# Kernel optimization log

Hardware: AMD Instinct MI355X
Metric: run time of the kernel (lower is better)

Reference implementation:

```python
import jax, jax.numpy as jnp
import numpy as np

N_NODES = 50000


def setup_inputs() -> dict:
    key = jax.random.key(0)
    ks = jax.random.split(key, 10)
    B, N, D, H, O = 2, N_NODES, 128, 128, 10
    x = jax.random.normal(ks[0], (B, N, D), dtype=jnp.float32)
    edge_index = jax.random.randint(ks[1], (2, 800000), 0, N, dtype=jnp.int32)
    s = lambda fan_in: 1.0 / np.sqrt(fan_in)
    W  = jax.random.uniform(ks[2], (D, H), jnp.float32, -s(D), s(D))
    b  = jnp.zeros((H,), jnp.float32)
    W1 = jax.random.uniform(ks[3], (H, H // 2), jnp.float32, -s(H), s(H))
    b1 = jnp.zeros((H // 2,), jnp.float32)
    W2 = jax.random.uniform(ks[4], (H // 2, H // 4), jnp.float32, -s(H // 2), s(H // 2))
    b2 = jnp.zeros((H // 4,), jnp.float32)
    W3 = jax.random.uniform(ks[5], (H // 4, O), jnp.float32, -s(H // 4), s(H // 4))
    b3 = jnp.zeros((O,), jnp.float32)
    return {"x": x, "edge_index": edge_index, "W": W, "b": b,
            "W1": W1, "b1": b1, "W2": W2, "b2": b2, "W3": W3, "b3": b3}


def reference(x, edge_index, W, b, W1, b1, W2, b2, W3, b3):
    # GraphConvolution (Kipf): support = x @ W; out[dst] += support[src]; + b
    src, dst = edge_index[0], edge_index[1]
    support = jnp.einsum("bnd,dh->bnh", x, W)          # [B, N, H]
    msgs = support[:, src, :]                            # [B, E, H] gather
    agg = jnp.zeros_like(support).at[:, dst, :].add(msgs)  # scatter-add
    h = jax.nn.gelu(agg + b, approximate=False)          # GELU (torch default erf)
    # dropout is identity at inference (training=False)
    h = jax.nn.relu(jnp.einsum("bnh,hk->bnk", h, W1) + b1)
    h = jax.nn.relu(jnp.einsum("bnk,km->bnm", h, W2) + b2)
    h = jnp.einsum("bnm,mo->bno", h, W3) + b3            # [B, N, O]
    return h.mean(axis=1)                                # [B, O]
```

## Files before the change

kernel.cpp:

```cpp
#include <hip/hip_runtime.h>
#include <math.h>

#define NN 50000
#define DD 128
#define HH 128
#define L1 64
#define L2 32
#define OO 10

typedef short v8s __attribute__((ext_vector_type(8)));
typedef float v4f __attribute__((ext_vector_type(4)));

__device__ __forceinline__ float bf2f_lo(unsigned u) { return __uint_as_float(u << 16); }
__device__ __forceinline__ float bf2f_hi(unsigned u) { return __uint_as_float(u & 0xffff0000u); }
__device__ __forceinline__ unsigned short f2bf(float f) {
    unsigned u = __float_as_uint(f);
    return (unsigned short)((u + 0x7fffu + ((u >> 16) & 1u)) >> 16);
}
__device__ __forceinline__ float gelu_f(float v) {
    return 0.5f * v * (1.f + erff(v * 0.70710678118654752f));
}

__global__ __launch_bounds__(256) void k_wprep(
    const float* __restrict__ W, const float* __restrict__ W1,
    const float* __restrict__ W2, unsigned short* __restrict__ wtb,
    unsigned short* __restrict__ w1tb, unsigned short* __restrict__ w2tb)
{
    int i = blockIdx.x * 256 + threadIdx.x;
    if (i < 128 * 136) {
        int n = i / 136, k = i % 136;
        wtb[i] = (k < DD) ? f2bf(W[k * HH + n]) : (unsigned short)0;
    } else if (i < 128 * 136 + 64 * 136) {
        int j = i - 128 * 136;
        int n = j / 136, k = j % 136;
        w1tb[j] = (k < HH) ? f2bf(W1[k * L1 + n]) : (unsigned short)0;
    } else if (i < 128 * 136 + 64 * 136 + 32 * 72) {
        int j = i - (128 * 136 + 64 * 136);
        int n = j / 72, k = j % 72;
        w2tb[j] = (k < L1) ? f2bf(W2[k * L2 + n]) : (unsigned short)0;
    }
}

__global__ __launch_bounds__(256) void k_xcvt(
    const float* __restrict__ x, unsigned short* __restrict__ xb,
    const int* __restrict__ ei, int* __restrict__ counts, int E)
{
    const int gid = blockIdx.x * 256 + threadIdx.x;
    const int stride = gridDim.x * 256;
    const int HALF = NN * 32;
    for (int idx = gid; idx < 2 * HALF; idx += stride) {
        const int b = (idx >= HALF) ? 1 : 0;
        const int j = idx - b * HALF;
        const int n = j >> 5;
        const int c4 = j & 31;
        const float4 v = *(const float4*)(x + ((size_t)b * NN + n) * DD + c4 * 4);
        ushort4 o;
        o.x = f2bf(v.x); o.y = f2bf(v.y); o.z = f2bf(v.z); o.w = f2bf(v.w);
        *(ushort4*)(xb + ((size_t)n * 2 + b) * DD + c4 * 4) = o;
    }
    for (int e = gid; e < E; e += stride)
        atomicAdd(&counts[ei[(size_t)E + e]], 1);
}

__global__ __launch_bounds__(1024) void k_scan1(
    const int* __restrict__ counts, int* __restrict__ offsets,
    int* __restrict__ blksum, int n)
{
    __shared__ int wsum[16], woff[16];
    const int tid = threadIdx.x, lane = tid & 63, wv = tid >> 6;
    const int i = blockIdx.x * 1024 + tid;
    int v = (i < n) ? counts[i] : 0;
    int x = v;
    #pragma unroll
    for (int d = 1; d < 64; d <<= 1) { int t = __shfl_up(x, d); if (lane >= d) x += t; }
    if (lane == 63) wsum[wv] = x;
    __syncthreads();
    if (wv == 0 && lane < 16) {
        int y = wsum[lane];
        #pragma unroll
        for (int d = 1; d < 16; d <<= 1) { int t = __shfl_up(y, d); if (lane >= d) y += t; }
        woff[lane] = y - wsum[lane];
        if (lane == 15) blksum[blockIdx.x] = y;
    }
    __syncthreads();
    if (i < n) offsets[i] = woff[wv] + (x - v);
}

__global__ __launch_bounds__(1024) void k_scan2(
    int* __restrict__ offsets, const int* __restrict__ blksum, int nblk, int n)
{
    __shared__ int base_sh, tot_sh;
    const int tid = threadIdx.x, lane = tid & 63, wv = tid >> 6;
    if (wv == 0) {
        int v = (lane < nblk) ? blksum[lane] : 0;
        int x = v;
        #pragma unroll
        for (int d = 1; d < 64; d <<= 1) { int t = __shfl_up(x, d); if (lane >= d) x += t; }
        int incl = __shfl(x, blockIdx.x);
        int own  = __shfl(v, blockIdx.x);
        int tot  = __shfl(x, nblk - 1);
        if (lane == 0) { base_sh = incl - own; tot_sh = tot; }
    }
    __syncthreads();
    const int i = blockIdx.x * 1024 + tid;
    if (i < n) offsets[i] += base_sh;
    if (blockIdx.x == nblk - 1 && tid == 0) offsets[n] = tot_sh;
}

__global__ __launch_bounds__(256) void k_bucket(
    const int* __restrict__ ei, const int* __restrict__ offsets,
    int* __restrict__ cursor, int* __restrict__ ss, int E)
{
    int e = blockIdx.x * 256 + threadIdx.x;
    if (e < E) {
        int d = ei[E + e];
        int pos = offsets[d] + atomicAdd(&cursor[d], 1);
        ss[pos] = ei[e];
    }
}

__global__ __launch_bounds__(256) void k_agg(
    const unsigned short* __restrict__ xb, const int* __restrict__ offsets,
    const int* __restrict__ ss, unsigned short* __restrict__ aggb, int nn)
{
    const int tid = threadIdx.x;
    const int lane = tid & 63;
    const int wv = tid >> 6;
    const int d = blockIdx.x * 4 + wv;
    if (d >= nn) return;
    const unsigned short* sp = xb + lane * 4;
    const int s0 = offsets[d], s1 = offsets[d + 1];
    float4 a = make_float4(0.f, 0.f, 0.f, 0.f);
    float4 a2 = make_float4(0.f, 0.f, 0.f, 0.f);
    int i = s0;
    for (; i + 4 <= s1; i += 4) {
        const int sA = ss[i], sB = ss[i + 1], sC = ss[i + 2], sD = ss[i + 3];
        const uint2 rA = *(const uint2*)(sp + (size_t)sA * 256);
        const uint2 rB = *(const uint2*)(sp + (size_t)sB * 256);
        const uint2 rC = *(const uint2*)(sp + (size_t)sC * 256);
        const uint2 rD = *(const uint2*)(sp + (size_t)sD * 256);
        a.x  += bf2f_lo(rA.x); a.y  += bf2f_hi(rA.x); a.z  += bf2f_lo(rA.y); a.w  += bf2f_hi(rA.y);
        a2.x += bf2f_lo(rB.x); a2.y += bf2f_hi(rB.x); a2.z += bf2f_lo(rB.y); a2.w += bf2f_hi(rB.y);
        a.x  += bf2f_lo(rC.x); a.y  += bf2f_hi(rC.x); a.z  += bf2f_lo(rC.y); a.w  += bf2f_hi(rC.y);
        a2.x += bf2f_lo(rD.x); a2.y += bf2f_hi(rD.x); a2.z += bf2f_lo(rD.y); a2.w += bf2f_hi(rD.y);
    }
    for (; i < s1; ++i) {
        const uint2 r = *(const uint2*)(sp + (size_t)ss[i] * 256);
        a.x += bf2f_lo(r.x); a.y += bf2f_hi(r.x); a.z += bf2f_lo(r.y); a.w += bf2f_hi(r.y);
    }
    a.x += a2.x; a.y += a2.y; a.z += a2.z; a.w += a2.w;
    ushort4 o;
    o.x = f2bf(a.x); o.y = f2bf(a.y); o.z = f2bf(a.z); o.w = f2bf(a.w);
    *(ushort4*)(aggb + (size_t)d * 256 + lane * 4) = o;
}

__global__ __launch_bounds__(512, 6) void k_mlp(
    const unsigned short* __restrict__ aggb, const unsigned short* __restrict__ wtb,
    const float* __restrict__ b0v,
    const unsigned short* __restrict__ w1tb, const float* __restrict__ b1v,
    const unsigned short* __restrict__ w2tb, const float* __restrict__ b2v,
    float* __restrict__ partials, int srows)
{
    __shared__ __align__(16) unsigned short wt1[64 * 136];
    __shared__ __align__(16) unsigned short wt2[32 * 72];
    __shared__ __align__(16) unsigned char upool[64 * 136 * 2];
    __shared__ __align__(16) unsigned short h1b[64 * 72];
    __shared__ float b0s[DD], b1s[L1], b2s[L2];
    __shared__ float oacc[64];
    unsigned short* xa  = (unsigned short*)upool;
    unsigned short* hsb = (unsigned short*)upool;
    float* h2p = (float*)upool;

    const int tid = threadIdx.x;
    const int row0 = blockIdx.x * 64;

    for (int u = tid * 4; u < 64 * 136; u += 2048)
        *(uint2*)(&wt1[u]) = *(const uint2*)(w1tb + u);
    for (int u = tid * 4; u < 32 * 72; u += 2048)
        *(uint2*)(&wt2[u]) = *(const uint2*)(w2tb + u);
    if (tid < DD) b0s[tid] = b0v[tid];
    if (tid < L1) b1s[tid] = b1v[tid];
    if (tid < L2) b2s[tid] = b2v[tid];
    if (tid < 64) oacc[tid] = 0.f;

    for (int u = tid * 8; u < 64 * DD; u += 4096) {
        const int r = u >> 7, c = u & 127;
        uint4 raw = make_uint4(0, 0, 0, 0);
        if (row0 + r < srows) raw = *(const uint4*)(aggb + (size_t)(row0 + r) * HH + c);
        *(uint4*)(&xa[r * 136 + c]) = raw;
    }
    __syncthreads();

    const int lane = tid & 63;
    const int w = tid >> 6;
    const int lm = lane & 15;
    const int q = lane >> 4;
    const int r1 = (w & 3) * 16;

    {
        const int c0 = (w >> 2) * 64;
        const unsigned short* wcol = wtb + (size_t)(c0 + lm) * 136;
        v4f acc[4];
        #pragma unroll
        for (int i = 0; i < 4; ++i) acc[i] = (v4f)(0.f);
        #pragma unroll
        for (int ks = 0; ks < 4; ++ks) {
            const int k0 = ks * 32 + q * 8;
            const v8s af = *(const v8s*)(&xa[(r1 + lm) * 136 + k0]);
            #pragma unroll
            for (int ct = 0; ct < 4; ++ct) {
                const v8s bf = *(const v8s*)(wcol + ct * 16 * 136 + k0);
                acc[ct] = __builtin_amdgcn_mfma_f32_16x16x32_bf16(af, bf, acc[ct], 0, 0, 0);
            }
        }
        __syncthreads();

        #pragma unroll
        for (int ct = 0; ct < 4; ++ct) {
            const int col = c0 + ct * 16 + lm;
            const float bias = b0s[col];
            #pragma unroll
            for (int r = 0; r < 4; ++r)
                hsb[(r1 + q * 4 + r) * 136 + col] = f2bf(gelu_f(acc[ct][r] + bias));
        }
    }
    __syncthreads();

    {
        const int c1 = (w >> 2) * 32;
        v4f a1[2];
        a1[0] = (v4f)(0.f); a1[1] = (v4f)(0.f);
        #pragma unroll
        for (int ks = 0; ks < 4; ++ks) {
            const int k0 = ks * 32 + q * 8;
            const v8s af = *(const v8s*)(&hsb[(r1 + lm) * 136 + k0]);
            #pragma unroll
            for (int ct = 0; ct < 2; ++ct) {
                const v8s bf = *(const v8s*)(&wt1[(c1 + ct * 16 + lm) * 136 + k0]);
                a1[ct] = __builtin_amdgcn_mfma_f32_16x16x32_bf16(af, bf, a1[ct], 0, 0, 0);
            }
        }
        #pragma unroll
        for (int ct = 0; ct < 2; ++ct) {
            const int col = c1 + ct * 16 + lm;
            const float bias = b1s[col];
            #pragma unroll
            for (int r = 0; r < 4; ++r)
                h1b[(r1 + q * 4 + r) * 72 + col] = f2bf(fmaxf(a1[ct][r] + bias, 0.f));
        }
    }
    __syncthreads();

    {
        const int c2 = (w >> 2) * 16;
        v4f a2 = (v4f)(0.f);
        #pragma unroll
        for (int ks = 0; ks < 2; ++ks) {
            const int k0 = ks * 32 + q * 8;
            const v8s af = *(const v8s*)(&h1b[(r1 + lm) * 72 + k0]);
            const v8s bf = *(const v8s*)(&wt2[(c2 + lm) * 72 + k0]);
            a2 = __builtin_amdgcn_mfma_f32_16x16x32_bf16(af, bf, a2, 0, 0, 0);
        }
        __syncthreads();
        const int col = c2 + lm;
        const float bias = b2s[col];
        #pragma unroll
        for (int r = 0; r < 4; ++r)
            h2p[(r1 + q * 4 + r) * 36 + col] = fmaxf(a2[r] + bias, 0.f);
    }
    __syncthreads();

    {
        const int c = tid & 31;
        const int g = tid >> 5;
        float p0 = 0.f, p1 = 0.f;
        #pragma unroll
        for (int i = 0; i < 4; ++i) {
            const int r = g * 4 + i;
            if (row0 + r < srows) {
                const float v = h2p[r * 36 + c];
                if (r & 1) p1 += v; else p0 += v;
            }
        }
        if (p0 != 0.f) atomicAdd(&oacc[c], p0);
        if (p1 != 0.f) atomicAdd(&oacc[32 + c], p1);
    }
    __syncthreads();
    if (tid < 64) partials[(size_t)blockIdx.x * 64 + tid] = oacc[tid];
}

__global__ __launch_bounds__(256) void k_scatter(
    const int* __restrict__ ei, const unsigned short* __restrict__ xb,
    float* __restrict__ aggf, int E)
{
    const int tid = threadIdx.x;
    const int eg = tid >> 6;
    const int lane = tid & 63;
    const int e = blockIdx.x * 4 + eg;
    if (e >= E) return;
    const int src = ei[e];
    const int dst = ei[E + e];
    const uint2 r = *(const uint2*)(xb + (size_t)src * 256 + lane * 4);
    float* ap = aggf + (size_t)dst * 256 + lane * 4;
    unsafeAtomicAdd(ap + 0, bf2f_lo(r.x));
    unsafeAtomicAdd(ap + 1, bf2f_hi(r.x));
    unsafeAtomicAdd(ap + 2, bf2f_lo(r.y));
    unsafeAtomicAdd(ap + 3, bf2f_hi(r.y));
}

__global__ __launch_bounds__(256) void k_cvt(
    const float* __restrict__ in, unsigned short* __restrict__ outb, int n)
{
    int i = blockIdx.x * 256 + threadIdx.x;
    if (i < n) outb[i] = f2bf(in[i]);
}

__global__ __launch_bounds__(256) void k_reduce(
    const float* __restrict__ partials, float* __restrict__ accum, int nblk)
{
    __shared__ float lsum[4][64];
    const int t = threadIdx.x & 63;
    const int w = threadIdx.x >> 6;
    float s = 0.f;
    for (int g = blockIdx.x * 4 + w; g < nblk; g += gridDim.x * 4)
        s += partials[(size_t)g * 64 + t];
    lsum[w][t] = s;
    __syncthreads();
    if (threadIdx.x < 64) {
        const float v = lsum[0][t] + lsum[1][t] + lsum[2][t] + lsum[3][t];
        unsafeAtomicAdd(&accum[t], v);
    }
}

__global__ __launch_bounds__(64) void k_final(
    const float* __restrict__ accum, const float* __restrict__ W3,
    const float* __restrict__ b3v, float* __restrict__ out)
{
    const int tid = threadIdx.x;
    if (tid < 2 * OO) {
        const int b = tid / OO, o = tid % OO;
        float acc = b3v[o];
        const float inv = 1.0f / (float)NN;
        #pragma unroll
        for (int j = 0; j < L2; ++j) acc += (accum[b * 32 + j] * inv) * W3[j * OO + o];
        out[tid] = acc;
    }
}

extern "C" void kernel_launch(void* const* d_in, const int* in_sizes, int n_in,
                              void* d_out, int out_size, void* d_ws, size_t ws_size,
                              hipStream_t stream) {
    const float* x  = (const float*)d_in[0];
    const int*   ei = (const int*)d_in[1];
    const float* W  = (const float*)d_in[2];
    const float* b0 = (const float*)d_in[3];
    const float* W1 = (const float*)d_in[4];
    const float* b1 = (const float*)d_in[5];
    const float* W2 = (const float*)d_in[6];
    const float* b2 = (const float*)d_in[7];
    const float* W3 = (const float*)d_in[8];
    const float* b3 = (const float*)d_in[9];
    float* out = (float*)d_out;

    const int E = in_sizes[1] / 2;
    const int rows = 2 * NN;
    const int nblk = (rows + 63) / 64;
    const int nsb = (NN + 1023) / 1024;
    const int wpn = 128 * 136 + 64 * 136 + 32 * 72;

    unsigned short* xb   = (unsigned short*)d_ws;
    unsigned short* aggb = xb + (size_t)rows * HH;
    float* partials = (float*)(aggb + (size_t)rows * HH);
    float* accum    = partials + (size_t)nblk * 64;
    int*   counts   = (int*)(accum + 64);
    int*   cursor   = counts + NN;
    int*   offsets  = cursor + NN;
    int*   blksum   = offsets + NN + 1;
    unsigned short* wtb  = (unsigned short*)(blksum + 64);
    unsigned short* w1tb = wtb + 128 * 136;
    unsigned short* w2tb = w1tb + 64 * 136;
    int*   ss       = (int*)(w2tb + 32 * 72);
    float* aggf     = (float*)(ss + E);
    const size_t need_csr = ((size_t)rows * HH * 2 + wpn) * sizeof(unsigned short)
                      + ((size_t)nblk * 64 + 64) * sizeof(float)
                      + ((size_t)NN * 3 + 1 + 64 + E) * sizeof(int);
    const size_t need_fb = need_csr + (size_t)rows * HH * sizeof(float);

    if (ws_size >= need_csr && nsb <= 64) {
        hipMemsetAsync(accum, 0, (64 + 2 * (size_t)NN) * sizeof(int), stream);
        k_wprep<<<dim3((wpn + 255) / 256), dim3(256), 0, stream>>>(W, W1, W2, wtb, w1tb, w2tb);
        k_xcvt<<<dim3(2048), dim3(256), 0, stream>>>(x, xb, ei, counts, E);
        k_scan1<<<dim3(nsb), dim3(1024), 0, stream>>>(counts, offsets, blksum, NN);
        k_scan2<<<dim3(nsb), dim3(1024), 0, stream>>>(offsets, blksum, nsb, NN);
        k_bucket<<<dim3((E + 255) / 256), dim3(256), 0, stream>>>(ei, offsets, cursor, ss, E);
        k_agg<<<dim3((NN + 3) / 4), dim3(256), 0, stream>>>(xb, offsets, ss, aggb, NN);
        k_mlp<<<dim3(nblk), dim3(512), 0, stream>>>(aggb, wtb, b0, w1tb, b1, w2tb, b2, partials, rows);
    } else if (ws_size >= need_fb) {
        hipMemsetAsync(accum, 0, 64 * sizeof(float), stream);
        hipMemsetAsync(aggf, 0, (size_t)rows * HH * sizeof(float), stream);
        k_wprep<<<dim3((wpn + 255) / 256), dim3(256), 0, stream>>>(W, W1, W2, wtb, w1tb, w2tb);
        k_xcvt<<<dim3(2048), dim3(256), 0, stream>>>(x, xb, ei, counts, 0);
        k_scatter<<<dim3((E + 3) / 4), dim3(256), 0, stream>>>(ei, xb, aggf, E);
        k_cvt<<<dim3((rows * HH + 255) / 256), dim3(256), 0, stream>>>(aggf, aggb, rows * HH);
        k_mlp<<<dim3(nblk), dim3(512), 0, stream>>>(aggb, wtb, b0, w1tb, b1, w2tb, b2, partials, rows);
    }

    k_reduce<<<dim3(64), dim3(256), 0, stream>>>(partials, accum, nblk);
    k_final<<<dim3(1), dim3(64), 0, stream>>>(accum, W3, b3, out);
}
```

Before: 281.8 us.

## Fuse CSR neighbor aggregation into MLP kernel and pre-swizzle weights into MFMA fragment order

Removes the separate aggregation kernel. The MLP kernel now gathers neighbor rows through the CSR lists directly into its shared-memory input tile, so the intermediate aggregated buffer is never written to and re-read from global memory. The weights are pre-packed into per-lane MFMA fragment order, so every layer reads its B operands with contiguous 16-byte global loads. This drops the shared-memory weight staging, which lowers LDS use and may raise occupancy. The costs are an irregular gather inside the MLP kernel, which can imbalance the blocks, and weight reads that now rely on cache hits.

```diff
diff --git a/kernel.cpp b/kernel.cpp
--- a/kernel.cpp
+++ b/kernel.cpp
@@ -8,6 +8,10 @@
 #define L2 32
 #define OO 10
 
+#define NW0 16384
+#define NW1 8192
+#define NW2 2048
+
 typedef short v8s __attribute__((ext_vector_type(8)));
 typedef float v4f __attribute__((ext_vector_type(4)));
 
@@ -17,27 +21,30 @@
     unsigned u = __float_as_uint(f);
     return (unsigned short)((u + 0x7fffu + ((u >> 16) & 1u)) >> 16);
 }
+__device__ __forceinline__ unsigned pack2(float lo, float hi) {
+    return (unsigned)f2bf(lo) | ((unsigned)f2bf(hi) << 16);
+}
 __device__ __forceinline__ float gelu_f(float v) {
     return 0.5f * v * (1.f + erff(v * 0.70710678118654752f));
 }
 
 __global__ __launch_bounds__(256) void k_wprep(
     const float* __restrict__ W, const float* __restrict__ W1,
-    const float* __restrict__ W2, unsigned short* __restrict__ wtb,
-    unsigned short* __restrict__ w1tb, unsigned short* __restrict__ w2tb)
+    const float* __restrict__ W2, unsigned short* __restrict__ wtp,
+    unsigned short* __restrict__ w1tp, unsigned short* __restrict__ w2tp)
 {
     int i = blockIdx.x * 256 + threadIdx.x;
-    if (i < 128 * 136) {
-        int n = i / 136, k = i % 136;
-        wtb[i] = (k < DD) ? f2bf(W[k * HH + n]) : (unsigned short)0;
-    } else if (i < 128 * 136 + 64 * 136) {
-        int j = i - 128 * 136;
-        int n = j / 136, k = j % 136;
-        w1tb[j] = (k < HH) ? f2bf(W1[k * L1 + n]) : (unsigned short)0;
-    } else if (i < 128 * 136 + 64 * 136 + 32 * 72) {
-        int j = i - (128 * 136 + 64 * 136);
-        int n = j / 72, k = j % 72;
-        w2tb[j] = (k < L1) ? f2bf(W2[k * L2 + n]) : (unsigned short)0;
+    if (i < NW0) {
+        const int e = i & 7, ln = (i >> 3) & 63, ks = (i >> 9) & 3, ct = i >> 11;
+        wtp[i] = f2bf(W[(ks * 32 + (ln >> 4) * 8 + e) * HH + ct * 16 + (ln & 15)]);
+    } else if (i < NW0 + NW1) {
+        const int j = i - NW0;
+        const int e = j & 7, ln = (j >> 3) & 63, ks = (j >> 9) & 3, ct = j >> 11;
+        w1tp[j] = f2bf(W1[(ks * 32 + (ln >> 4) * 8 + e) * L1 + ct * 16 + (ln & 15)]);
+    } else if (i < NW0 + NW1 + NW2) {
+        const int j = i - NW0 - NW1;
+        const int e = j & 7, ln = (j >> 3) & 63, ks = (j >> 9) & 1, ct = j >> 10;
+        w2tp[j] = f2bf(W2[(ks * 32 + (ln >> 4) * 8 + e) * L2 + ct * 16 + (ln & 15)]);
     }
 }
 
@@ -119,50 +126,15 @@
     }
 }
 
-__global__ __launch_bounds__(256) void k_agg(
-    const unsigned short* __restrict__ xb, const int* __restrict__ offsets,
-    const int* __restrict__ ss, unsigned short* __restrict__ aggb, int nn)
-{
-    const int tid = threadIdx.x;
-    const int lane = tid & 63;
-    const int wv = tid >> 6;
-    const int d = blockIdx.x * 4 + wv;
-    if (d >= nn) return;
-    const unsigned short* sp = xb + lane * 4;
-    const int s0 = offsets[d], s1 = offsets[d + 1];
-    float4 a = make_float4(0.f, 0.f, 0.f, 0.f);
-    float4 a2 = make_float4(0.f, 0.f, 0.f, 0.f);
-    int i = s0;
-    for (; i + 4 <= s1; i += 4) {
-        const int sA = ss[i], sB = ss[i + 1], sC = ss[i + 2], sD = ss[i + 3];
-        const uint2 rA = *(const uint2*)(sp + (size_t)sA * 256);
-        const uint2 rB = *(const uint2*)(sp + (size_t)sB * 256);
-        const uint2 rC = *(const uint2*)(sp + (size_t)sC * 256);
-        const uint2 rD = *(const uint2*)(sp + (size_t)sD * 256);
-        a.x  += bf2f_lo(rA.x); a.y  += bf2f_hi(rA.x); a.z  += bf2f_lo(rA.y); a.w  += bf2f_hi(rA.y);
-        a2.x += bf2f_lo(rB.x); a2.y += bf2f_hi(rB.x); a2.z += bf2f_lo(rB.y); a2.w += bf2f_hi(rB.y);
-        a.x  += bf2f_lo(rC.x); a.y  += bf2f_hi(rC.x); a.z  += bf2f_lo(rC.y); a.w  += bf2f_hi(rC.y);
-        a2.x += bf2f_lo(rD.x); a2.y += bf2f_hi(rD.x); a2.z += bf2f_lo(rD.y); a2.w += bf2f_hi(rD.y);
-    }
-    for (; i < s1; ++i) {
-        const uint2 r = *(const uint2*)(sp + (size_t)ss[i] * 256);
-        a.x += bf2f_lo(r.x); a.y += bf2f_hi(r.x); a.z += bf2f_lo(r.y); a.w += bf2f_hi(r.y);
-    }
-    a.x += a2.x; a.y += a2.y; a.z += a2.z; a.w += a2.w;
-    ushort4 o;
-    o.x = f2bf(a.x); o.y = f2bf(a.y); o.z = f2bf(a.z); o.w = f2bf(a.w);
-    *(ushort4*)(aggb + (size_t)d * 256 + lane * 4) = o;
-}
-
-__global__ __launch_bounds__(512, 6) void k_mlp(
-    const unsigned short* __restrict__ aggb, const unsigned short* __restrict__ wtb,
-    const float* __restrict__ b0v,
-    const unsigned short* __restrict__ w1tb, const float* __restrict__ b1v,
-    const unsigned short* __restrict__ w2tb, const float* __restrict__ b2v,
+template<bool FUSED>
+__global__ __launch_bounds__(512, 6) void k_mlp_t(
+    const unsigned short* __restrict__ src,
+    const int* __restrict__ offsets, const int* __restrict__ ss,
+    const unsigned short* __restrict__ wtp, const float* __restrict__ b0v,
+    const unsigned short* __restrict__ w1tp, const float* __restrict__ b1v,
+    const unsigned short* __restrict__ w2tp, const float* __restrict__ b2v,
     float* __restrict__ partials, int srows)
 {
-    __shared__ __align__(16) unsigned short wt1[64 * 136];
-    __shared__ __align__(16) unsigned short wt2[32 * 72];
     __shared__ __align__(16) unsigned char upool[64 * 136 * 2];
     __shared__ __align__(16) unsigned short h1b[64 * 72];
     __shared__ float b0s[DD], b1s[L1], b2s[L2];
@@ -173,33 +145,85 @@
 
     const int tid = threadIdx.x;
     const int row0 = blockIdx.x * 64;
-
-    for (int u = tid * 4; u < 64 * 136; u += 2048)
-        *(uint2*)(&wt1[u]) = *(const uint2*)(w1tb + u);
-    for (int u = tid * 4; u < 32 * 72; u += 2048)
-        *(uint2*)(&wt2[u]) = *(const uint2*)(w2tb + u);
+    const int lane = tid & 63;
+    const int w = tid >> 6;
+
     if (tid < DD) b0s[tid] = b0v[tid];
     if (tid < L1) b1s[tid] = b1v[tid];
     if (tid < L2) b2s[tid] = b2v[tid];
     if (tid < 64) oacc[tid] = 0.f;
 
-    for (int u = tid * 8; u < 64 * DD; u += 4096) {
-        const int r = u >> 7, c = u & 127;
-        uint4 raw = make_uint4(0, 0, 0, 0);
-        if (row0 + r < srows) raw = *(const uint4*)(aggb + (size_t)(row0 + r) * HH + c);
-        *(uint4*)(&xa[r * 136 + c]) = raw;
-    }
-    __syncthreads();
-
-    const int lane = tid & 63;
-    const int w = tid >> 6;
+    if (FUSED) {
+        const int sel = (lane < 32) ? 0 : 1;
+        const int co = (lane & 31) * 8;
+        #pragma unroll
+        for (int j = 0; j < 4; ++j) {
+            const int ln = w * 4 + j;
+            const int d = blockIdx.x * 32 + ln;
+            const int s0 = (d < NN) ? offsets[d] : 0;
+            const int s1 = (d < NN) ? offsets[d + 1] : 0;
+            float a[8];
+            #pragma unroll
+            for (int t = 0; t < 8; ++t) a[t] = 0.f;
+            int i = s0;
+            for (; i + 4 <= s1; i += 4) {
+                const int sA = ss[i + sel];
+                const int sB = ss[i + 2 + sel];
+                const uint4 ra = *(const uint4*)(src + (size_t)sA * 256 + co);
+                const uint4 rb = *(const uint4*)(src + (size_t)sB * 256 + co);
+                a[0] += bf2f_lo(ra.x); a[1] += bf2f_hi(ra.x);
+                a[2] += bf2f_lo(ra.y); a[3] += bf2f_hi(ra.y);
+                a[4] += bf2f_lo(ra.z); a[5] += bf2f_hi(ra.z);
+                a[6] += bf2f_lo(ra.w); a[7] += bf2f_hi(ra.w);
+                a[0] += bf2f_lo(rb.x); a[1] += bf2f_hi(rb.x);
+                a[2] += bf2f_lo(rb.y); a[3] += bf2f_hi(rb.y);
+                a[4] += bf2f_lo(rb.z); a[5] += bf2f_hi(rb.z);
+                a[6] += bf2f_lo(rb.w); a[7] += bf2f_hi(rb.w);
+            }
+            if (i + 2 <= s1) {
+                const int sA = ss[i + sel];
+                const uint4 ra = *(const uint4*)(src + (size_t)sA * 256 + co);
+                a[0] += bf2f_lo(ra.x); a[1] += bf2f_hi(ra.x);
+                a[2] += bf2f_lo(ra.y); a[3] += bf2f_hi(ra.y);
+                a[4] += bf2f_lo(ra.z); a[5] += bf2f_hi(ra.z);
+                a[6] += bf2f_lo(ra.w); a[7] += bf2f_hi(ra.w);
+                i += 2;
+            }
+            if (i < s1 && lane < 32) {
+                const int sA = ss[i];
+                const uint4 ra = *(const uint4*)(src + (size_t)sA * 256 + co);
+                a[0] += bf2f_lo(ra.x); a[1] += bf2f_hi(ra.x);
+                a[2] += bf2f_lo(ra.y); a[3] += bf2f_hi(ra.y);
+                a[4] += bf2f_lo(ra.z); a[5] += bf2f_hi(ra.z);
+                a[6] += bf2f_lo(ra.w); a[7] += bf2f_hi(ra.w);
+            }
+            #pragma unroll
+            for (int t = 0; t < 8; ++t) a[t] += __shfl_xor(a[t], 32);
+            if (lane < 32) {
+                const int tr = ln * 2 + (lane >> 4);
+                const int col = (lane & 15) * 8;
+                uint4 o;
+                o.x = pack2(a[0], a[1]); o.y = pack2(a[2], a[3]);
+                o.z = pack2(a[4], a[5]); o.w = pack2(a[6], a[7]);
+                *(uint4*)(&xa[tr * 136 + col]) = o;
+            }
+        }
+    } else {
+        for (int u = tid * 8; u < 64 * DD; u += 4096) {
+            const int r = u >> 7, c = u & 127;
+            uint4 raw = make_uint4(0, 0, 0, 0);
+            if (row0 + r < srows) raw = *(const uint4*)(src + (size_t)(row0 + r) * HH + c);
+            *(uint4*)(&xa[r * 136 + c]) = raw;
+        }
+    }
+    __syncthreads();
+
     const int lm = lane & 15;
     const int q = lane >> 4;
     const int r1 = (w & 3) * 16;
+    const int ch = w >> 2;
 
     {
-        const int c0 = (w >> 2) * 64;
-        const unsigned short* wcol = wtb + (size_t)(c0 + lm) * 136;
         v4f acc[4];
         #pragma unroll
         for (int i = 0; i < 4; ++i) acc[i] = (v4f)(0.f);
@@ -209,7 +233,8 @@
             const v8s af = *(const v8s*)(&xa[(r1 + lm) * 136 + k0]);
             #pragma unroll
             for (int ct = 0; ct < 4; ++ct) {
-                const v8s bf = *(const v8s*)(wcol + ct * 16 * 136 + k0);
+                const int ctg = ch * 4 + ct;
+                const v8s bf = *(const v8s*)(wtp + ((size_t)(ctg * 4 + ks) * 64 + lane) * 8);
                 acc[ct] = __builtin_amdgcn_mfma_f32_16x16x32_bf16(af, bf, acc[ct], 0, 0, 0);
             }
         }
@@ -217,7 +242,7 @@
 
         #pragma unroll
         for (int ct = 0; ct < 4; ++ct) {
-            const int col = c0 + ct * 16 + lm;
+            const int col = ch * 64 + ct * 16 + lm;
             const float bias = b0s[col];
             #pragma unroll
             for (int r = 0; r < 4; ++r)
@@ -227,7 +252,6 @@
     __syncthreads();
 
     {
-        const int c1 = (w >> 2) * 32;
         v4f a1[2];
         a1[0] = (v4f)(0.f); a1[1] = (v4f)(0.f);
         #pragma unroll
@@ -236,13 +260,14 @@
             const v8s af = *(const v8s*)(&hsb[(r1 + lm) * 136 + k0]);
             #pragma unroll
             for (int ct = 0; ct < 2; ++ct) {
-                const v8s bf = *(const v8s*)(&wt1[(c1 + ct * 16 + lm) * 136 + k0]);
+                const int ctg = ch * 2 + ct;
+                const v8s bf = *(const v8s*)(w1tp + ((size_t)(ctg * 4 + ks) * 64 + lane) * 8);
                 a1[ct] = __builtin_amdgcn_mfma_f32_16x16x32_bf16(af, bf, a1[ct], 0, 0, 0);
             }
         }
         #pragma unroll
         for (int ct = 0; ct < 2; ++ct) {
-            const int col = c1 + ct * 16 + lm;
+            const int col = ch * 32 + ct * 16 + lm;
             const float bias = b1s[col];
             #pragma unroll
             for (int r = 0; r < 4; ++r)
@@ -252,17 +277,16 @@
     __syncthreads();
 
     {
-        const int c2 = (w >> 2) * 16;
         v4f a2 = (v4f)(0.f);
         #pragma unroll
         for (int ks = 0; ks < 2; ++ks) {
             const int k0 = ks * 32 + q * 8;
             const v8s af = *(const v8s*)(&h1b[(r1 + lm) * 72 + k0]);
-            const v8s bf = *(const v8s*)(&wt2[(c2 + lm) * 72 + k0]);
+            const v8s bf = *(const v8s*)(w2tp + ((size_t)(ch * 2 + ks) * 64 + lane) * 8);
             a2 = __builtin_amdgcn_mfma_f32_16x16x32_bf16(af, bf, a2, 0, 0, 0);
         }
         __syncthreads();
-        const int col = c2 + lm;
+        const int col = ch * 16 + lm;
         const float bias = b2s[col];
         #pragma unroll
         for (int r = 0; r < 4; ++r)
@@ -366,7 +390,7 @@
     const int rows = 2 * NN;
     const int nblk = (rows + 63) / 64;
     const int nsb = (NN + 1023) / 1024;
-    const int wpn = 128 * 136 + 64 * 136 + 32 * 72;
+    const int wpn = NW0 + NW1 + NW2;
 
     unsigned short* xb   = (unsigned short*)d_ws;
     unsigned short* aggb = xb + (size_t)rows * HH;
@@ -376,33 +400,34 @@
     int*   cursor   = counts + NN;
     int*   offsets  = cursor + NN;
     int*   blksum   = offsets + NN + 1;
-    unsigned short* wtb  = (unsigned short*)(blksum + 64);
-    unsigned short* w1tb = wtb + 128 * 136;
-    unsigned short* w2tb = w1tb + 64 * 136;
-    int*   ss       = (int*)(w2tb + 32 * 72);
+    unsigned short* wtp = (unsigned short*)(((uintptr_t)(blksum + 64) + 15) & ~(uintptr_t)15);
+    unsigned short* w1tp = wtp + NW0;
+    unsigned short* w2tp = w1tp + NW1;
+    int*   ss       = (int*)(w2tp + NW2);
     float* aggf     = (float*)(ss + E);
     const size_t need_csr = ((size_t)rows * HH * 2 + wpn) * sizeof(unsigned short)
                       + ((size_t)nblk * 64 + 64) * sizeof(float)
-                      + ((size_t)NN * 3 + 1 + 64 + E) * sizeof(int);
+                      + ((size_t)NN * 3 + 1 + 64 + E) * sizeof(int) + 16;
     const size_t need_fb = need_csr + (size_t)rows * HH * sizeof(float);
 
     if (ws_size >= need_csr && nsb <= 64) {
         hipMemsetAsync(accum, 0, (64 + 2 * (size_t)NN) * sizeof(int), stream);
-        k_wprep<<<dim3((wpn + 255) / 256), dim3(256), 0, stream>>>(W, W1, W2, wtb, w1tb, w2tb);
+        k_wprep<<<dim3((wpn + 255) / 256), dim3(256), 0, stream>>>(W, W1, W2, wtp, w1tp, w2tp);
         k_xcvt<<<dim3(2048), dim3(256), 0, stream>>>(x, xb, ei, counts, E);
         k_scan1<<<dim3(nsb), dim3(1024), 0, stream>>>(counts, offsets, blksum, NN);
         k_scan2<<<dim3(nsb), dim3(1024), 0, stream>>>(offsets, blksum, nsb, NN);
         k_bucket<<<dim3((E + 255) / 256), dim3(256), 0, stream>>>(ei, offsets, cursor, ss, E);
-        k_agg<<<dim3((NN + 3) / 4), dim3(256), 0, stream>>>(xb, offsets, ss, aggb, NN);
-        k_mlp<<<dim3(nblk), dim3(512), 0, stream>>>(aggb, wtb, b0, w1tb, b1, w2tb, b2, partials, rows);
+        k_mlp_t<true><<<dim3(nblk), dim3(512), 0, stream>>>(
+            xb, offsets, ss, wtp, b0, w1tp, b1, w2tp, b2, partials, rows);
     } else if (ws_size >= need_fb) {
         hipMemsetAsync(accum, 0, 64 * sizeof(float), stream);
         hipMemsetAsync(aggf, 0, (size_t)rows * HH * sizeof(float), stream);
-        k_wprep<<<dim3((wpn + 255) / 256), dim3(256), 0, stream>>>(W, W1, W2, wtb, w1tb, w2tb);
+        k_wprep<<<dim3((wpn + 255) / 256), dim3(256), 0, stream>>>(W, W1, W2, wtp, w1tp, w2tp);
         k_xcvt<<<dim3(2048), dim3(256), 0, stream>>>(x, xb, ei, counts, 0);
         k_scatter<<<dim3((E + 3) / 4), dim3(256), 0, stream>>>(ei, xb, aggf, E);
         k_cvt<<<dim3((rows * HH + 255) / 256), dim3(256), 0, stream>>>(aggf, aggb, rows * HH);
-        k_mlp<<<dim3(nblk), dim3(512), 0, stream>>>(aggb, wtb, b0, w1tb, b1, w2tb, b2, partials, rows);
+        k_mlp_t<false><<<dim3(nblk), dim3(512), 0, stream>>>(
+            aggb, offsets, ss, wtp, b0, w1tp, b1, w2tp, b2, partials, rows);
     }
 
     k_reduce<<<dim3(64), dim3(256), 0, stream>>>(partials, accum, nblk);
```

After: 263.8 us, median of 2. -6.4%, faster.
